# Optimization experiments

Measured on AMD Instinct MI355X. Metric: run time of the kernel, lower is better.

The kernel has to match this reference:

```python
import jax, jax.numpy as jnp
import numpy as np

BLOCK = 32          # QLinearLPBQ block_size
W_BITS = 4          # low-precision blockwise weight quantization
ACT_BITS = 16       # ActivationQDQ(bits=16)


def act_qdq(x):
    # per-tensor symmetric 16-bit fake quant-dequant (dynamic absmax scale)
    qmax = 2.0 ** (ACT_BITS - 1) - 1.0  # 32767
    scale = jnp.maximum(jnp.max(jnp.abs(x)) / qmax, 1e-12)
    return jnp.clip(jnp.round(x / scale), -qmax - 1.0, qmax) * scale


def fixed_qdq_u16(x):
    # FixedActivationQDQ: scale = 1/65536, zero_point = 0, unsigned 16-bit grid
    scale = 1.0 / 65536.0
    return jnp.clip(jnp.round(x / scale), 0.0, 65535.0) * scale


def lpbq_dequant(w):
    # blockwise (per output row, per 32-wide input block) 4-bit fake quant-dequant
    O, I = w.shape
    qmax = 2.0 ** (W_BITS - 1) - 1.0  # 7
    wb = w.reshape(O, I // BLOCK, BLOCK)
    s = jnp.maximum(jnp.max(jnp.abs(wb), axis=-1, keepdims=True) / qmax, 1e-12)
    wq = jnp.clip(jnp.round(wb / s), -qmax - 1.0, qmax) * s
    return wq.reshape(O, I)


def setup_inputs() -> dict:
    key = jax.random.key(0)
    k1, k2, k3, k4 = jax.random.split(key, 4)
    B, S, H, I = 2, 4096, 1024, 3072
    x = jax.random.normal(k1, (B, S, H), jnp.float32)
    w_gate = jax.random.normal(k2, (I, H), jnp.float32) * 0.02
    w_up = jax.random.normal(k3, (I, H), jnp.float32) * 0.02
    w_down = jax.random.normal(k4, (H, I), jnp.float32) * 0.02
    return {"x": x, "w_gate": w_gate, "w_up": w_up, "w_down": w_down}


def reference(x, w_gate, w_up, w_down):
    # x: [B, S, H]
    x = act_qdq(x)                                        # up_proj_input_qdq
    up = act_qdq(x @ lpbq_dequant(w_up).T)                # up_proj + output qdq -> [B,S,I]
    gate = act_qdq(x @ lpbq_dequant(w_gate).T)            # gate_proj + output qdq
    sig = fixed_qdq_u16(jax.nn.sigmoid(gate))             # sigmoid on fixed u16 grid
    gate = act_qdq(gate * sig)                            # SiLU (x*sigmoid) + qdq
    o = act_qdq(gate * up)                                # down_proj_input_qdq
    return o @ lpbq_dequant(w_down).T                     # [B, S, H]
```

## Files before the change

kernel.cpp:

```cpp
#include <hip/hip_runtime.h>
#include <hip/hip_bf16.h>
#include <stdint.h>


#define M_ROWS 8192
#define H_DIM 1024
#define I_DIM 3072

typedef unsigned short u16;
typedef unsigned int u32;
typedef __attribute__((ext_vector_type(8))) short bf16x8;
typedef __attribute__((ext_vector_type(4))) float f32x4;

#define WAITVM(n) asm volatile("s_waitcnt vmcnt(" #n ")" ::: "memory")
#define BAR()                                   \
  do {                                          \
    asm volatile("" ::: "memory");              \
    __builtin_amdgcn_s_barrier();               \
    asm volatile("" ::: "memory");              \
  } while (0)

__device__ __forceinline__ float bf2f(u16 v) { return __uint_as_float(((u32)v) << 16); }
__device__ __forceinline__ u16 f2bf(float f) {
  u32 u = __float_as_uint(f);
  u32 r = (u + 0x7fffu + ((u >> 16) & 1u)) >> 16;
  return (u16)r;
}
__device__ __forceinline__ float qdq16i(float x, float inv, float s) {
  float q = rintf(x * inv);
  q = fminf(fmaxf(q, -32768.f), 32767.f);
  return q * s;
}
__device__ __forceinline__ float sigq(float g) {
  float sig = __builtin_amdgcn_rcpf(1.f + __expf(-g));
  return fminf(fmaxf(rintf(sig * 65536.f), 0.f), 65535.f) * (1.f / 65536.f);
}

__device__ __forceinline__ float scale_read(const u32* __restrict__ scal, int s) {
  u32 m = 0;
#pragma unroll
  for (int j = 0; j < 16; ++j) m = max(m, scal[j * 16 + s]);
  return fmaxf(__uint_as_float(m) / 32767.f, 1e-12f);
}

__device__ __forceinline__ void load_lds16(const u16* g, u16* lds) {
  __builtin_amdgcn_global_load_lds(
      (const __attribute__((address_space(1))) u32*)g,
      (__attribute__((address_space(3))) u32*)lds, 16, 0, 0);
}

__device__ __forceinline__ void block_amax_atomic(float mx, u32* scal, int s) {
#pragma unroll
  for (int off = 32; off; off >>= 1) mx = fmaxf(mx, __shfl_xor(mx, off));
  __shared__ float red[4];
  const int lane = threadIdx.x & 63, wave = threadIdx.x >> 6;
  if (lane == 0) red[wave] = mx;
  __syncthreads();
  if (threadIdx.x == 0) {
    float m = fmaxf(fmaxf(red[0], red[1]), fmaxf(red[2], red[3]));
    atomicMax(scal + (blockIdx.x & 15) * 16 + s, __float_as_uint(m));
  }
}

__device__ __forceinline__ void block_amax4(float a, float b, float c, float d,
                                            u32* __restrict__ scal) {
#pragma unroll
  for (int off = 32; off; off >>= 1) {
    a = fmaxf(a, __shfl_xor(a, off));
    b = fmaxf(b, __shfl_xor(b, off));
    c = fmaxf(c, __shfl_xor(c, off));
    d = fmaxf(d, __shfl_xor(d, off));
  }
  __shared__ float red4[4][4];
  const int lane = threadIdx.x & 63, wave = threadIdx.x >> 6;
  if (lane == 0) {
    red4[0][wave] = a;
    red4[1][wave] = b;
    red4[2][wave] = c;
    red4[3][wave] = d;
  }
  __syncthreads();
  if (threadIdx.x == 0) {
    u32* base = scal + (blockIdx.x & 15) * 16;
#pragma unroll
    for (int s = 0; s < 4; ++s) {
      float m = fmaxf(fmaxf(red4[s][0], red4[s][1]), fmaxf(red4[s][2], red4[s][3]));
      atomicMax(base + 1 + s, __float_as_uint(m));
    }
  }
}

__global__ void __launch_bounds__(256, 2) kgemm1(const u16* __restrict__ xq,
                                                 const u16* __restrict__ wcat,
                                                 u16* __restrict__ up, u16* __restrict__ gh,
                                                 u32* __restrict__ scal) {
  __shared__ __align__(16) u16 smem[36864];
  const int tileN = blockIdx.x * 128;
  const int tileM = blockIdx.y * 128;
  const int tid = threadIdx.x;
  const int lane = tid & 63, wave = tid >> 6;
  const int wm = wave >> 1, wn = wave & 1;
  const int quad = lane >> 4, mrow = lane & 15;

  const u16* Ablk = xq + (size_t)tileM * H_DIM;
  const u16* Bublk = wcat + (size_t)tileN * H_DIM;
  const u16* Bgblk = wcat + (size_t)(I_DIM + tileN) * H_DIM;

  int goff[2], loff[2];
#pragma unroll
  for (int t = 0; t < 2; ++t) {
    const int c = tid + 256 * t;
    const int r = c >> 2, q = c & 3;
    goff[t] = r * H_DIM + ((q ^ ((r >> 1) & 3)) << 3);
    loff[t] = c << 3;
  }
  const int pc = (quad ^ ((mrow >> 1) & 3)) << 3;
  int aoff[4], boff[4];
#pragma unroll
  for (int i = 0; i < 4; ++i) {
    aoff[i] = (wm * 64 + i * 16 + mrow) * 32 + pc;
    boff[i] = (wn * 64 + i * 16 + mrow) * 32 + pc;
  }

  f32x4 accg[4][4], accu[4][4];
#pragma unroll
  for (int i = 0; i < 4; ++i)
#pragma unroll
    for (int j = 0; j < 4; ++j) {
      accg[i][j] = (f32x4){0.f, 0.f, 0.f, 0.f};
      accu[i][j] = (f32x4){0.f, 0.f, 0.f, 0.f};
    }

  auto stage = [&](int k0, int bb) {
    u16* d = smem + bb;
#pragma unroll
    for (int t = 0; t < 2; ++t) load_lds16(Ablk + k0 + goff[t], d + loff[t]);
#pragma unroll
    for (int t = 0; t < 2; ++t) load_lds16(Bublk + k0 + goff[t], d + 4096 + loff[t]);
#pragma unroll
    for (int t = 0; t < 2; ++t) load_lds16(Bgblk + k0 + goff[t], d + 8192 + loff[t]);
  };
  auto compute = [&](int bb) {
    const u16* As = smem + bb;
    const u16* Bus = As + 4096;
    const u16* Bgs = As + 8192;
    bf16x8 af[4];
#pragma unroll
    for (int i = 0; i < 4; ++i) af[i] = *(const bf16x8*)&As[aoff[i]];
#pragma unroll
    for (int j = 0; j < 4; ++j) {
      bf16x8 b = *(const bf16x8*)&Bus[boff[j]];
#pragma unroll
      for (int i = 0; i < 4; ++i)
        accu[i][j] = __builtin_amdgcn_mfma_f32_16x16x32_bf16(af[i], b, accu[i][j], 0, 0, 0);
    }
#pragma unroll
    for (int j = 0; j < 4; ++j) {
      bf16x8 b = *(const bf16x8*)&Bgs[boff[j]];
#pragma unroll
      for (int i = 0; i < 4; ++i)
        accg[i][j] = __builtin_amdgcn_mfma_f32_16x16x32_bf16(af[i], b, accg[i][j], 0, 0, 0);
    }
  };

  stage(0, 0);
  stage(32, 12288);
  stage(64, 24576);
  WAITVM(12);
  BAR();

  int bb = 0;
#pragma unroll 1
  for (int t = 0; t < 29; ++t) {
    compute(bb);
    BAR();
    stage((t + 3) * 32, bb);
    WAITVM(12);
    BAR();
    bb = (bb == 24576) ? 0 : bb + 12288;
  }
  compute(bb); BAR(); WAITVM(6); BAR(); bb = (bb == 24576) ? 0 : bb + 12288;
  compute(bb); BAR(); WAITVM(0); BAR(); bb = (bb == 24576) ? 0 : bb + 12288;
  compute(bb);

  const int rb = (lane >> 4) * 4, cb = lane & 15;
  const int erow = lane >> 2, echk = lane & 3;
  u16* gstage = smem + wave * 1152;
  u16* ustage = smem + 12288 + wave * 1152;
  const u16* grb = gstage + erow * 72;
  const u16* urb = ustage + erow * 72;
  float mxg = 0.f, mxu = 0.f, mxh = 0.f, mxo = 0.f;
#pragma unroll
  for (int i = 0; i < 4; ++i) {
    __syncthreads();
#pragma unroll
    for (int j = 0; j < 4; ++j)
#pragma unroll
      for (int r = 0; r < 4; ++r) {
        float g = accg[i][j][r];
        float u = accu[i][j][r];
        mxg = fmaxf(mxg, fabsf(g));
        mxu = fmaxf(mxu, fabsf(u));
        float ha = g * sigq(g);
        mxh = fmaxf(mxh, fabsf(ha));
        mxo = fmaxf(mxo, fabsf(ha * u));
        gstage[(rb + r) * 72 + j * 16 + cb] = f2bf(g);
        ustage[(rb + r) * 72 + j * 16 + cb] = f2bf(u);
      }
    __syncthreads();
    uint4 g0 = *(const uint4*)(grb + echk * 8);
    uint4 g1 = *(const uint4*)(grb + (echk + 4) * 8);
    uint4 u0 = *(const uint4*)(urb + echk * 8);
    uint4 u1 = *(const uint4*)(urb + (echk + 4) * 8);
    size_t grow = (size_t)(tileM + wm * 64 + i * 16 + erow) * I_DIM + (tileN + wn * 64);
    *(uint4*)(gh + grow + echk * 8) = g0;
    *(uint4*)(gh + grow + (echk + 4) * 8) = g1;
    *(uint4*)(up + grow + echk * 8) = u0;
    *(uint4*)(up + grow + (echk + 4) * 8) = u1;
  }
  block_amax4(mxu, mxg, mxh, mxo, scal);
}

__global__ void __launch_bounds__(256, 2) kgemm2(const u16* __restrict__ oq,
                                                 const u16* __restrict__ wdq,
                                                 float* __restrict__ out) {
  __shared__ __align__(16) u16 smem[32768];
  const int tileN = blockIdx.x * 128;
  const int tileM = blockIdx.y * 128;
  const int tid = threadIdx.x;
  const int lane = tid & 63, wave = tid >> 6;
  const int wm = wave >> 1, wn = wave & 1;
  const int quad = lane >> 4, mrow = lane & 15;

  const u16* Ablk = oq + (size_t)tileM * I_DIM;
  const u16* Bblk = wdq + (size_t)tileN * I_DIM;

  int goff[2], loff[2];
#pragma unroll
  for (int t = 0; t < 2; ++t) {
    const int c = tid + 256 * t;
    const int r = c >> 2, q = c & 3;
    goff[t] = r * I_DIM + ((q ^ ((r >> 1) & 3)) << 3);
    loff[t] = c << 3;
  }
  const int pc = (quad ^ ((mrow >> 1) & 3)) << 3;
  int aoff[4], boff[4];
#pragma unroll
  for (int i = 0; i < 4; ++i) {
    aoff[i] = (wm * 64 + i * 16 + mrow) * 32 + pc;
    boff[i] = (wn * 64 + i * 16 + mrow) * 32 + pc;
  }

  f32x4 acc[4][4];
#pragma unroll
  for (int i = 0; i < 4; ++i)
#pragma unroll
    for (int j = 0; j < 4; ++j) acc[i][j] = (f32x4){0.f, 0.f, 0.f, 0.f};

  auto stage = [&](int k0, int bb) {
    u16* d = smem + bb;
#pragma unroll
    for (int t = 0; t < 2; ++t) load_lds16(Ablk + k0 + goff[t], d + loff[t]);
#pragma unroll
    for (int t = 0; t < 2; ++t) load_lds16(Bblk + k0 + goff[t], d + 4096 + loff[t]);
  };
  auto compute = [&](int bb) {
    const u16* As = smem + bb;
    const u16* Bs = As + 4096;
    bf16x8 af[4];
#pragma unroll
    for (int i = 0; i < 4; ++i) af[i] = *(const bf16x8*)&As[aoff[i]];
#pragma unroll
    for (int j = 0; j < 4; ++j) {
      bf16x8 b = *(const bf16x8*)&Bs[boff[j]];
#pragma unroll
      for (int i = 0; i < 4; ++i)
        acc[i][j] = __builtin_amdgcn_mfma_f32_16x16x32_bf16(af[i], b, acc[i][j], 0, 0, 0);
    }
  };

  stage(0, 0);
  stage(32, 8192);
  stage(64, 16384);
  stage(96, 24576);
  WAITVM(12);
  BAR();

  int bb = 0;
#pragma unroll 1
  for (int t = 0; t < 92; ++t) {
    compute(bb);
    BAR();
    stage((t + 4) * 32, bb);
    WAITVM(12);
    BAR();
    bb = (bb + 8192) & 32767;
  }
  compute(bb); BAR(); WAITVM(8); BAR(); bb = (bb + 8192) & 32767;
  compute(bb); BAR(); WAITVM(4); BAR(); bb = (bb + 8192) & 32767;
  compute(bb); BAR(); WAITVM(0); BAR(); bb = (bb + 8192) & 32767;
  compute(bb);

  const int rb = (lane >> 4) * 4, cb = lane & 15;
#pragma unroll
  for (int i = 0; i < 4; ++i) {
#pragma unroll
    for (int j = 0; j < 4; ++j) {
      size_t base = (size_t)(tileM + wm * 64 + i * 16 + rb) * H_DIM +
                    (size_t)(tileN + wn * 64 + j * 16 + cb);
#pragma unroll
      for (int r = 0; r < 4; ++r) out[base + (size_t)r * H_DIM] = acc[i][j][r];
    }
  }
}

__global__ void __launch_bounds__(256) kprep(const float* __restrict__ x,
                                             const float* __restrict__ wu,
                                             const float* __restrict__ wg,
                                             const float* __restrict__ wdn,
                                             u16* __restrict__ wcat, u16* __restrict__ wdq,
                                             u32* __restrict__ scal) {
  if (blockIdx.x < 1024) {
    const float4* x4 = (const float4*)x;
    const int n4 = (M_ROWS * H_DIM) / 4;
    float mx = 0.f;
    for (int i = blockIdx.x * 256 + threadIdx.x; i < n4; i += 1024 * 256) {
      float4 v = x4[i];
      mx = fmaxf(fmaxf(fabsf(v.x), fabsf(v.y)), fmaxf(fmaxf(fabsf(v.z), fabsf(v.w)), mx));
    }
    block_amax_atomic(mx, scal, 0);
    return;
  }
  const int gid = (blockIdx.x - 1024) * 256 + threadIdx.x;
  const int unit = gid >> 3, l8 = gid & 7;
  const float* src;
  u16* dst;
  int u;
  if (unit < 98304)       { src = wu;  dst = wcat;            u = unit; }
  else if (unit < 196608) { src = wg;  dst = wcat + 3145728;  u = unit - 98304; }
  else                    { src = wdn; dst = wdq;             u = unit - 196608; }
  const size_t off = (size_t)u * 32 + (size_t)l8 * 4;
  float4 v = *(const float4*)(src + off);
  float m = fmaxf(fmaxf(fabsf(v.x), fabsf(v.y)), fmaxf(fabsf(v.z), fabsf(v.w)));
  m = fmaxf(m, __shfl_xor(m, 1));
  m = fmaxf(m, __shfl_xor(m, 2));
  m = fmaxf(m, __shfl_xor(m, 4));
  const float s = fmaxf(m / 7.0f, 1e-12f);
  const float inv = 1.0f / s;
  float vv[4] = {v.x, v.y, v.z, v.w};
  u16 o[4];
#pragma unroll
  for (int e = 0; e < 4; ++e) {
    float q = rintf(vv[e] * inv);
    q = fminf(fmaxf(q, -8.f), 7.f);
    o[e] = f2bf(q * s);
  }
  *(ushort4*)(dst + off) = make_ushort4(o[0], o[1], o[2], o[3]);
}

__global__ void __launch_bounds__(256) kqdqx(const float4* __restrict__ x,
                                             ushort4* __restrict__ xq,
                                             const u32* __restrict__ scal) {
  const float s = scale_read(scal, 0);
  const float inv = 1.0f / s;
  const int i = blockIdx.x * 256 + threadIdx.x;
  float4 v = x[i];
  ushort4 o;
  o.x = f2bf(qdq16i(v.x, inv, s));
  o.y = f2bf(qdq16i(v.y, inv, s));
  o.z = f2bf(qdq16i(v.z, inv, s));
  o.w = f2bf(qdq16i(v.w, inv, s));
  xq[i] = o;
}

#define GH4 ((M_ROWS * I_DIM) / 8)
#define EW_BLOCKS 2048

__global__ void __launch_bounds__(256) kmulo(uint4* __restrict__ gh, const uint4* __restrict__ up,
                                             u32* __restrict__ scal) {
  const float sg = scale_read(scal, 2), ig = 1.0f / sg;
  const float sh = scale_read(scal, 3), ih = 1.0f / sh;
  const float su = scale_read(scal, 1), iu = 1.0f / su;
  const float so = scale_read(scal, 4), io = 1.0f / so;
  for (int i = blockIdx.x * 256 + threadIdx.x; i < GH4; i += EW_BLOCKS * 256) {
    union { uint4 v; u16 us[8]; } a, b;
    a.v = gh[i];
    b.v = up[i];
#pragma unroll
    for (int e = 0; e < 8; ++e) {
      float g = qdq16i(bf2f(a.us[e]), ig, sg);
      float h = g * sigq(g);
      float o = qdq16i(h, ih, sh) * qdq16i(bf2f(b.us[e]), iu, su);
      a.us[e] = f2bf(qdq16i(o, io, so));
    }
    gh[i] = a.v;
  }
}

extern "C" void kernel_launch(void* const* d_in, const int* in_sizes, int n_in,
                              void* d_out, int out_size, void* d_ws, size_t ws_size,
                              hipStream_t stream) {
  (void)in_sizes; (void)n_in; (void)out_size; (void)ws_size;
  const float* x   = (const float*)d_in[0];
  const float* wg  = (const float*)d_in[1];
  const float* wu  = (const float*)d_in[2];
  const float* wdn = (const float*)d_in[3];
  float* out = (float*)d_out;
  char* ws = (char*)d_ws;

  u32* scal = (u32*)ws;
  u16* xq   = (u16*)(ws + 1024);
  u16* wcat = xq + (size_t)M_ROWS * H_DIM;
  u16* wdq  = wcat + (size_t)2 * I_DIM * H_DIM;
  u16* up   = wdq + (size_t)H_DIM * I_DIM;
  u16* gh   = up + (size_t)M_ROWS * I_DIM;

  hipMemsetAsync(scal, 0, 1024, stream);
  kprep<<<1024 + 9216, 256, 0, stream>>>(x, wu, wg, wdn, wcat, wdq, scal);
  kqdqx<<<(M_ROWS * H_DIM) / 4 / 256, 256, 0, stream>>>((const float4*)x, (ushort4*)xq, scal);
  kgemm1<<<dim3(24, 64), 256, 0, stream>>>(xq, wcat, up, gh, scal);
  kmulo<<<EW_BLOCKS, 256, 0, stream>>>((uint4*)gh, (const uint4*)up, scal);
  kgemm2<<<dim3(8, 64), 256, 0, stream>>>(gh, wdq, out);
}
```

Measured before the change: 323.1 us.

## Interleave up/gate weights and use 256x256 tiles with 8 waves in gemm1

The up and gate weight rows are interleaved in 16-row groups, so gemm1 runs as a single 256x256-tile GEMM over the combined 6144-wide output using 512 threads. This doubles A-tile reuse and halves the number of blocks. The intermediate is stored as one interleaved buffer, and the elementwise kernel and gemm2's A loads are remapped to read the interleaved layout in place. The larger LDS footprint and the 128 accumulator floats per thread may lower occupancy or cause register spills.

```diff
diff --git a/kernel.cpp b/kernel.cpp
--- a/kernel.cpp
+++ b/kernel.cpp
@@ -62,8 +62,8 @@
   }
 }
 
-__device__ __forceinline__ void block_amax4(float a, float b, float c, float d,
-                                            u32* __restrict__ scal) {
+__device__ __forceinline__ void block_amax4_8w(float a, float b, float c, float d,
+                                               u32* __restrict__ scal) {
 #pragma unroll
   for (int off = 32; off; off >>= 1) {
     a = fmaxf(a, __shfl_xor(a, off));
@@ -71,7 +71,7 @@
     c = fmaxf(c, __shfl_xor(c, off));
     d = fmaxf(d, __shfl_xor(d, off));
   }
-  __shared__ float red4[4][4];
+  __shared__ float red4[4][8];
   const int lane = threadIdx.x & 63, wave = threadIdx.x >> 6;
   if (lane == 0) {
     red4[0][wave] = a;
@@ -84,89 +84,76 @@
     u32* base = scal + (blockIdx.x & 15) * 16;
 #pragma unroll
     for (int s = 0; s < 4; ++s) {
-      float m = fmaxf(fmaxf(red4[s][0], red4[s][1]), fmaxf(red4[s][2], red4[s][3]));
+      float m = 0.f;
+#pragma unroll
+      for (int w = 0; w < 8; ++w) m = fmaxf(m, red4[s][w]);
       atomicMax(base + 1 + s, __float_as_uint(m));
     }
   }
 }
 
-__global__ void __launch_bounds__(256, 2) kgemm1(const u16* __restrict__ xq,
+__global__ void __launch_bounds__(512, 2) kgemm1(const u16* __restrict__ xq,
                                                  const u16* __restrict__ wcat,
-                                                 u16* __restrict__ up, u16* __restrict__ gh,
+                                                 u16* __restrict__ gu,
                                                  u32* __restrict__ scal) {
-  __shared__ __align__(16) u16 smem[36864];
-  const int tileN = blockIdx.x * 128;
-  const int tileM = blockIdx.y * 128;
+  __shared__ __align__(16) u16 smem[49152];
+  const int tileN = blockIdx.x * 256;
+  const int tileM = blockIdx.y * 256;
   const int tid = threadIdx.x;
   const int lane = tid & 63, wave = tid >> 6;
-  const int wm = wave >> 1, wn = wave & 1;
+  const int wm = wave >> 2, wn = wave & 3;
   const int quad = lane >> 4, mrow = lane & 15;
 
   const u16* Ablk = xq + (size_t)tileM * H_DIM;
-  const u16* Bublk = wcat + (size_t)tileN * H_DIM;
-  const u16* Bgblk = wcat + (size_t)(I_DIM + tileN) * H_DIM;
+  const u16* Bblk = wcat + (size_t)tileN * H_DIM;
 
   int goff[2], loff[2];
 #pragma unroll
   for (int t = 0; t < 2; ++t) {
-    const int c = tid + 256 * t;
+    const int c = tid + 512 * t;
     const int r = c >> 2, q = c & 3;
     goff[t] = r * H_DIM + ((q ^ ((r >> 1) & 3)) << 3);
     loff[t] = c << 3;
   }
   const int pc = (quad ^ ((mrow >> 1) & 3)) << 3;
-  int aoff[4], boff[4];
-#pragma unroll
-  for (int i = 0; i < 4; ++i) {
-    aoff[i] = (wm * 64 + i * 16 + mrow) * 32 + pc;
-    boff[i] = (wn * 64 + i * 16 + mrow) * 32 + pc;
-  }
-
-  f32x4 accg[4][4], accu[4][4];
-#pragma unroll
-  for (int i = 0; i < 4; ++i)
-#pragma unroll
-    for (int j = 0; j < 4; ++j) {
-      accg[i][j] = (f32x4){0.f, 0.f, 0.f, 0.f};
-      accu[i][j] = (f32x4){0.f, 0.f, 0.f, 0.f};
-    }
+  int arow[8], brow[4];
+#pragma unroll
+  for (int i = 0; i < 8; ++i) arow[i] = (wm * 128 + i * 16 + mrow) * 32 + pc;
+#pragma unroll
+  for (int j = 0; j < 4; ++j) brow[j] = (wn * 64 + j * 16 + mrow) * 32 + pc;
+
+  f32x4 acc[8][4];
+#pragma unroll
+  for (int i = 0; i < 8; ++i)
+#pragma unroll
+    for (int j = 0; j < 4; ++j) acc[i][j] = (f32x4){0.f, 0.f, 0.f, 0.f};
 
   auto stage = [&](int k0, int bb) {
     u16* d = smem + bb;
 #pragma unroll
     for (int t = 0; t < 2; ++t) load_lds16(Ablk + k0 + goff[t], d + loff[t]);
 #pragma unroll
-    for (int t = 0; t < 2; ++t) load_lds16(Bublk + k0 + goff[t], d + 4096 + loff[t]);
-#pragma unroll
-    for (int t = 0; t < 2; ++t) load_lds16(Bgblk + k0 + goff[t], d + 8192 + loff[t]);
+    for (int t = 0; t < 2; ++t) load_lds16(Bblk + k0 + goff[t], d + 8192 + loff[t]);
   };
   auto compute = [&](int bb) {
     const u16* As = smem + bb;
-    const u16* Bus = As + 4096;
-    const u16* Bgs = As + 8192;
-    bf16x8 af[4];
-#pragma unroll
-    for (int i = 0; i < 4; ++i) af[i] = *(const bf16x8*)&As[aoff[i]];
+    const u16* Bs = As + 8192;
+    bf16x8 af[8];
+#pragma unroll
+    for (int i = 0; i < 8; ++i) af[i] = *(const bf16x8*)&As[arow[i]];
 #pragma unroll
     for (int j = 0; j < 4; ++j) {
-      bf16x8 b = *(const bf16x8*)&Bus[boff[j]];
-#pragma unroll
-      for (int i = 0; i < 4; ++i)
-        accu[i][j] = __builtin_amdgcn_mfma_f32_16x16x32_bf16(af[i], b, accu[i][j], 0, 0, 0);
-    }
-#pragma unroll
-    for (int j = 0; j < 4; ++j) {
-      bf16x8 b = *(const bf16x8*)&Bgs[boff[j]];
-#pragma unroll
-      for (int i = 0; i < 4; ++i)
-        accg[i][j] = __builtin_amdgcn_mfma_f32_16x16x32_bf16(af[i], b, accg[i][j], 0, 0, 0);
+      bf16x8 b = *(const bf16x8*)&Bs[brow[j]];
+#pragma unroll
+      for (int i = 0; i < 8; ++i)
+        acc[i][j] = __builtin_amdgcn_mfma_f32_16x16x32_bf16(af[i], b, acc[i][j], 0, 0, 0);
     }
   };
 
   stage(0, 0);
-  stage(32, 12288);
-  stage(64, 24576);
-  WAITVM(12);
+  stage(32, 16384);
+  stage(64, 32768);
+  WAITVM(8);
   BAR();
 
   int bb = 0;
@@ -175,53 +162,48 @@
     compute(bb);
     BAR();
     stage((t + 3) * 32, bb);
-    WAITVM(12);
+    WAITVM(8);
     BAR();
-    bb = (bb == 24576) ? 0 : bb + 12288;
-  }
-  compute(bb); BAR(); WAITVM(6); BAR(); bb = (bb == 24576) ? 0 : bb + 12288;
-  compute(bb); BAR(); WAITVM(0); BAR(); bb = (bb == 24576) ? 0 : bb + 12288;
+    bb = (bb == 32768) ? 0 : bb + 16384;
+  }
+  compute(bb); BAR(); WAITVM(4); BAR(); bb = (bb == 32768) ? 0 : bb + 16384;
+  compute(bb); BAR(); WAITVM(0); BAR(); bb = (bb == 32768) ? 0 : bb + 16384;
   compute(bb);
 
   const int rb = (lane >> 4) * 4, cb = lane & 15;
   const int erow = lane >> 2, echk = lane & 3;
-  u16* gstage = smem + wave * 1152;
-  u16* ustage = smem + 12288 + wave * 1152;
-  const u16* grb = gstage + erow * 72;
-  const u16* urb = ustage + erow * 72;
+  u16* wstage = smem + wave * 1152;
+  const u16* wrb = wstage + erow * 72;
   float mxg = 0.f, mxu = 0.f, mxh = 0.f, mxo = 0.f;
 #pragma unroll
-  for (int i = 0; i < 4; ++i) {
+  for (int i = 0; i < 8; ++i) {
     __syncthreads();
 #pragma unroll
-    for (int j = 0; j < 4; ++j)
+    for (int jp = 0; jp < 4; jp += 2)
 #pragma unroll
       for (int r = 0; r < 4; ++r) {
-        float g = accg[i][j][r];
-        float u = accu[i][j][r];
+        float u = acc[i][jp][r];
+        float g = acc[i][jp + 1][r];
+        mxu = fmaxf(mxu, fabsf(u));
         mxg = fmaxf(mxg, fabsf(g));
-        mxu = fmaxf(mxu, fabsf(u));
         float ha = g * sigq(g);
         mxh = fmaxf(mxh, fabsf(ha));
         mxo = fmaxf(mxo, fabsf(ha * u));
-        gstage[(rb + r) * 72 + j * 16 + cb] = f2bf(g);
-        ustage[(rb + r) * 72 + j * 16 + cb] = f2bf(u);
+        wstage[(rb + r) * 72 + jp * 16 + cb] = f2bf(u);
+        wstage[(rb + r) * 72 + (jp + 1) * 16 + cb] = f2bf(g);
       }
     __syncthreads();
-    uint4 g0 = *(const uint4*)(grb + echk * 8);
-    uint4 g1 = *(const uint4*)(grb + (echk + 4) * 8);
-    uint4 u0 = *(const uint4*)(urb + echk * 8);
-    uint4 u1 = *(const uint4*)(urb + (echk + 4) * 8);
-    size_t grow = (size_t)(tileM + wm * 64 + i * 16 + erow) * I_DIM + (tileN + wn * 64);
-    *(uint4*)(gh + grow + echk * 8) = g0;
-    *(uint4*)(gh + grow + (echk + 4) * 8) = g1;
-    *(uint4*)(up + grow + echk * 8) = u0;
-    *(uint4*)(up + grow + (echk + 4) * 8) = u1;
-  }
-  block_amax4(mxu, mxg, mxh, mxo, scal);
-}
-
-__global__ void __launch_bounds__(256, 2) kgemm2(const u16* __restrict__ oq,
+    uint4 v0 = *(const uint4*)(wrb + echk * 8);
+    uint4 v1 = *(const uint4*)(wrb + (echk + 4) * 8);
+    size_t grow = (size_t)(tileM + wm * 128 + i * 16 + erow) * (2 * I_DIM) +
+                  (tileN + wn * 64);
+    *(uint4*)(gu + grow + echk * 8) = v0;
+    *(uint4*)(gu + grow + (echk + 4) * 8) = v1;
+  }
+  block_amax4_8w(mxu, mxg, mxh, mxo, scal);
+}
+
+__global__ void __launch_bounds__(256, 2) kgemm2(const u16* __restrict__ gu,
                                                  const u16* __restrict__ wdq,
                                                  float* __restrict__ out) {
   __shared__ __align__(16) u16 smem[32768];
@@ -232,15 +214,17 @@
   const int wm = wave >> 1, wn = wave & 1;
   const int quad = lane >> 4, mrow = lane & 15;
 
-  const u16* Ablk = oq + (size_t)tileM * I_DIM;
+  const u16* Ablk = gu + (size_t)tileM * (2 * I_DIM);
   const u16* Bblk = wdq + (size_t)tileN * I_DIM;
 
-  int goff[2], loff[2];
+  int goffA[2], goffB[2], loff[2];
 #pragma unroll
   for (int t = 0; t < 2; ++t) {
     const int c = tid + 256 * t;
     const int r = c >> 2, q = c & 3;
-    goff[t] = r * I_DIM + ((q ^ ((r >> 1) & 3)) << 3);
+    const int l = q ^ ((r >> 1) & 3);
+    goffA[t] = r * (2 * I_DIM) + ((l >> 1) << 5) + ((l & 1) << 3);
+    goffB[t] = r * I_DIM + (l << 3);
     loff[t] = c << 3;
   }
   const int pc = (quad ^ ((mrow >> 1) & 3)) << 3;
@@ -260,9 +244,9 @@
   auto stage = [&](int k0, int bb) {
     u16* d = smem + bb;
 #pragma unroll
-    for (int t = 0; t < 2; ++t) load_lds16(Ablk + k0 + goff[t], d + loff[t]);
-#pragma unroll
-    for (int t = 0; t < 2; ++t) load_lds16(Bblk + k0 + goff[t], d + 4096 + loff[t]);
+    for (int t = 0; t < 2; ++t) load_lds16(Ablk + 2 * k0 + goffA[t], d + loff[t]);
+#pragma unroll
+    for (int t = 0; t < 2; ++t) load_lds16(Bblk + k0 + goffB[t], d + 4096 + loff[t]);
   };
   auto compute = [&](int bb) {
     const u16* As = smem + bb;
@@ -335,12 +319,23 @@
   const int unit = gid >> 3, l8 = gid & 7;
   const float* src;
   u16* dst;
-  int u;
-  if (unit < 98304)       { src = wu;  dst = wcat;            u = unit; }
-  else if (unit < 196608) { src = wg;  dst = wcat + 3145728;  u = unit - 98304; }
-  else                    { src = wdn; dst = wdq;             u = unit - 196608; }
-  const size_t off = (size_t)u * 32 + (size_t)l8 * 4;
-  float4 v = *(const float4*)(src + off);
+  size_t soff, doff;
+  if (unit < 196608) {
+    const int head = unit < 98304 ? 0 : 1;
+    const int u = head ? unit - 98304 : unit;
+    src = head ? wg : wu;
+    dst = wcat;
+    const int c = u >> 5, blk = u & 31;
+    const int n = ((c >> 4) << 5) + (head << 4) + (c & 15);
+    soff = (size_t)u * 32 + l8 * 4;
+    doff = (size_t)n * 1024 + blk * 32 + l8 * 4;
+  } else {
+    const int u = unit - 196608;
+    src = wdn;
+    dst = wdq;
+    soff = doff = (size_t)u * 32 + l8 * 4;
+  }
+  float4 v = *(const float4*)(src + soff);
   float m = fmaxf(fmaxf(fabsf(v.x), fabsf(v.y)), fmaxf(fabsf(v.z), fabsf(v.w)));
   m = fmaxf(m, __shfl_xor(m, 1));
   m = fmaxf(m, __shfl_xor(m, 2));
@@ -355,7 +350,7 @@
     q = fminf(fmaxf(q, -8.f), 7.f);
     o[e] = f2bf(q * s);
   }
-  *(ushort4*)(dst + off) = make_ushort4(o[0], o[1], o[2], o[3]);
+  *(ushort4*)(dst + doff) = make_ushort4(o[0], o[1], o[2], o[3]);
 }
 
 __global__ void __launch_bounds__(256) kqdqx(const float4* __restrict__ x,
@@ -373,27 +368,36 @@
   xq[i] = o;
 }
 
-#define GH4 ((M_ROWS * I_DIM) / 8)
 #define EW_BLOCKS 2048
 
-__global__ void __launch_bounds__(256) kmulo(uint4* __restrict__ gh, const uint4* __restrict__ up,
+__global__ void __launch_bounds__(256) kmulo(uint4* __restrict__ gu4,
                                              u32* __restrict__ scal) {
   const float sg = scale_read(scal, 2), ig = 1.0f / sg;
   const float sh = scale_read(scal, 3), ih = 1.0f / sh;
   const float su = scale_read(scal, 1), iu = 1.0f / su;
   const float so = scale_read(scal, 4), io = 1.0f / so;
-  for (int i = blockIdx.x * 256 + threadIdx.x; i < GH4; i += EW_BLOCKS * 256) {
-    union { uint4 v; u16 us[8]; } a, b;
-    a.v = gh[i];
-    b.v = up[i];
+  const int NG = M_ROWS * 192;
+  for (int idx = blockIdx.x * 256 + threadIdx.x; idx < NG; idx += EW_BLOCKS * 256) {
+    const int m = idx / 192, b = idx - m * 192;
+    const int i0 = m * 768 + b * 4;
+    union { uint4 v; u16 us[8]; } u0, u1, g0, g1;
+    u0.v = gu4[i0];
+    u1.v = gu4[i0 + 1];
+    g0.v = gu4[i0 + 2];
+    g1.v = gu4[i0 + 3];
 #pragma unroll
     for (int e = 0; e < 8; ++e) {
-      float g = qdq16i(bf2f(a.us[e]), ig, sg);
+      float g = qdq16i(bf2f(g0.us[e]), ig, sg);
       float h = g * sigq(g);
-      float o = qdq16i(h, ih, sh) * qdq16i(bf2f(b.us[e]), iu, su);
-      a.us[e] = f2bf(qdq16i(o, io, so));
-    }
-    gh[i] = a.v;
+      float o = qdq16i(h, ih, sh) * qdq16i(bf2f(u0.us[e]), iu, su);
+      u0.us[e] = f2bf(qdq16i(o, io, so));
+      float g2 = qdq16i(bf2f(g1.us[e]), ig, sg);
+      float h2 = g2 * sigq(g2);
+      float o2 = qdq16i(h2, ih, sh) * qdq16i(bf2f(u1.us[e]), iu, su);
+      u1.us[e] = f2bf(qdq16i(o2, io, so));
+    }
+    gu4[i0] = u0.v;
+    gu4[i0 + 1] = u1.v;
   }
 }
 
@@ -412,13 +416,12 @@
   u16* xq   = (u16*)(ws + 1024);
   u16* wcat = xq + (size_t)M_ROWS * H_DIM;
   u16* wdq  = wcat + (size_t)2 * I_DIM * H_DIM;
-  u16* up   = wdq + (size_t)H_DIM * I_DIM;
-  u16* gh   = up + (size_t)M_ROWS * I_DIM;
+  u16* gu   = wdq + (size_t)H_DIM * I_DIM;
 
   hipMemsetAsync(scal, 0, 1024, stream);
   kprep<<<1024 + 9216, 256, 0, stream>>>(x, wu, wg, wdn, wcat, wdq, scal);
   kqdqx<<<(M_ROWS * H_DIM) / 4 / 256, 256, 0, stream>>>((const float4*)x, (ushort4*)xq, scal);
-  kgemm1<<<dim3(24, 64), 256, 0, stream>>>(xq, wcat, up, gh, scal);
-  kmulo<<<EW_BLOCKS, 256, 0, stream>>>((uint4*)gh, (const uint4*)up, scal);
-  kgemm2<<<dim3(8, 64), 256, 0, stream>>>(gh, wdq, out);
-}
+  kgemm1<<<dim3(24, 32), 512, 0, stream>>>(xq, wcat, gu, scal);
+  kmulo<<<EW_BLOCKS, 256, 0, stream>>>((uint4*)gu, scal);
+  kgemm2<<<dim3(8, 64), 256, 0, stream>>>(gu, wdq, out);
+}
```

After: 385.7 us. +19.4%, slower.

## Enlarge down-proj GEMM tile to 256x128 with three-stage LDS pipeline

Applied to the files above, without the earlier changes.

The down-projection GEMM now computes a 256x128 output tile per block instead of 128x128, so each wave accumulates an 8x4 grid of MFMA tiles and each loaded B fragment is reused across twice as many A rows. To fit in shared memory, the LDS ring drops from four stages to three, with 24 KB per stage. The grid is halved to 256 blocks. The accumulators double to 128 floats per thread, which raises register pressure against the 2-blocks-per-SM launch bound, and the shallower prefetch may expose more memory latency. With only 256 blocks, the work may also spread unevenly across the CUs.

```diff
diff --git a/kernel.cpp b/kernel.cpp
--- a/kernel.cpp
+++ b/kernel.cpp
@@ -224,9 +224,9 @@
 __global__ void __launch_bounds__(256, 2) kgemm2(const u16* __restrict__ oq,
                                                  const u16* __restrict__ wdq,
                                                  float* __restrict__ out) {
-  __shared__ __align__(16) u16 smem[32768];
+  __shared__ __align__(16) u16 smem[36864];
   const int tileN = blockIdx.x * 128;
-  const int tileM = blockIdx.y * 128;
+  const int tileM = blockIdx.y * 256;
   const int tid = threadIdx.x;
   const int lane = tid & 63, wave = tid >> 6;
   const int wm = wave >> 1, wn = wave & 1;
@@ -235,78 +235,82 @@
   const u16* Ablk = oq + (size_t)tileM * I_DIM;
   const u16* Bblk = wdq + (size_t)tileN * I_DIM;
 
-  int goff[2], loff[2];
+  int goffA[4], loffA[4], goffB[2], loffB[2];
+#pragma unroll
+  for (int t = 0; t < 4; ++t) {
+    const int c = tid + 256 * t;
+    const int r = c >> 2, q = c & 3;
+    goffA[t] = r * I_DIM + ((q ^ ((r >> 1) & 3)) << 3);
+    loffA[t] = c << 3;
+  }
 #pragma unroll
   for (int t = 0; t < 2; ++t) {
     const int c = tid + 256 * t;
     const int r = c >> 2, q = c & 3;
-    goff[t] = r * I_DIM + ((q ^ ((r >> 1) & 3)) << 3);
-    loff[t] = c << 3;
+    goffB[t] = r * I_DIM + ((q ^ ((r >> 1) & 3)) << 3);
+    loffB[t] = c << 3;
   }
   const int pc = (quad ^ ((mrow >> 1) & 3)) << 3;
-  int aoff[4], boff[4];
-#pragma unroll
-  for (int i = 0; i < 4; ++i) {
-    aoff[i] = (wm * 64 + i * 16 + mrow) * 32 + pc;
-    boff[i] = (wn * 64 + i * 16 + mrow) * 32 + pc;
-  }
-
-  f32x4 acc[4][4];
-#pragma unroll
-  for (int i = 0; i < 4; ++i)
+  int aoff[8], boff[4];
+#pragma unroll
+  for (int i = 0; i < 8; ++i) aoff[i] = (wm * 128 + i * 16 + mrow) * 32 + pc;
+#pragma unroll
+  for (int j = 0; j < 4; ++j) boff[j] = (wn * 64 + j * 16 + mrow) * 32 + pc;
+
+  f32x4 acc[8][4];
+#pragma unroll
+  for (int i = 0; i < 8; ++i)
 #pragma unroll
     for (int j = 0; j < 4; ++j) acc[i][j] = (f32x4){0.f, 0.f, 0.f, 0.f};
 
   auto stage = [&](int k0, int bb) {
     u16* d = smem + bb;
 #pragma unroll
-    for (int t = 0; t < 2; ++t) load_lds16(Ablk + k0 + goff[t], d + loff[t]);
-#pragma unroll
-    for (int t = 0; t < 2; ++t) load_lds16(Bblk + k0 + goff[t], d + 4096 + loff[t]);
+    for (int t = 0; t < 4; ++t) load_lds16(Ablk + k0 + goffA[t], d + loffA[t]);
+#pragma unroll
+    for (int t = 0; t < 2; ++t) load_lds16(Bblk + k0 + goffB[t], d + 8192 + loffB[t]);
   };
   auto compute = [&](int bb) {
     const u16* As = smem + bb;
-    const u16* Bs = As + 4096;
-    bf16x8 af[4];
-#pragma unroll
-    for (int i = 0; i < 4; ++i) af[i] = *(const bf16x8*)&As[aoff[i]];
+    const u16* Bs = As + 8192;
+    bf16x8 af[8];
+#pragma unroll
+    for (int i = 0; i < 8; ++i) af[i] = *(const bf16x8*)&As[aoff[i]];
 #pragma unroll
     for (int j = 0; j < 4; ++j) {
       bf16x8 b = *(const bf16x8*)&Bs[boff[j]];
 #pragma unroll
-      for (int i = 0; i < 4; ++i)
+      for (int i = 0; i < 8; ++i)
         acc[i][j] = __builtin_amdgcn_mfma_f32_16x16x32_bf16(af[i], b, acc[i][j], 0, 0, 0);
     }
   };
 
   stage(0, 0);
-  stage(32, 8192);
-  stage(64, 16384);
-  stage(96, 24576);
+  stage(32, 12288);
+  stage(64, 24576);
   WAITVM(12);
   BAR();
 
   int bb = 0;
 #pragma unroll 1
-  for (int t = 0; t < 92; ++t) {
+  for (int t = 0; t < 93; ++t) {
     compute(bb);
     BAR();
-    stage((t + 4) * 32, bb);
+    stage((t + 3) * 32, bb);
     WAITVM(12);
     BAR();
-    bb = (bb + 8192) & 32767;
-  }
-  compute(bb); BAR(); WAITVM(8); BAR(); bb = (bb + 8192) & 32767;
-  compute(bb); BAR(); WAITVM(4); BAR(); bb = (bb + 8192) & 32767;
-  compute(bb); BAR(); WAITVM(0); BAR(); bb = (bb + 8192) & 32767;
+    bb = (bb == 24576) ? 0 : bb + 12288;
+  }
+  compute(bb); BAR(); WAITVM(6); BAR(); bb = (bb == 24576) ? 0 : bb + 12288;
+  compute(bb); BAR(); WAITVM(0); BAR(); bb = (bb == 24576) ? 0 : bb + 12288;
   compute(bb);
 
   const int rb = (lane >> 4) * 4, cb = lane & 15;
 #pragma unroll
-  for (int i = 0; i < 4; ++i) {
+  for (int i = 0; i < 8; ++i) {
 #pragma unroll
     for (int j = 0; j < 4; ++j) {
-      size_t base = (size_t)(tileM + wm * 64 + i * 16 + rb) * H_DIM +
+      size_t base = (size_t)(tileM + wm * 128 + i * 16 + rb) * H_DIM +
                     (size_t)(tileN + wn * 64 + j * 16 + cb);
 #pragma unroll
       for (int r = 0; r < 4; ++r) out[base + (size_t)r * H_DIM] = acc[i][j][r];
@@ -420,5 +424,5 @@
   kqdqx<<<(M_ROWS * H_DIM) / 4 / 256, 256, 0, stream>>>((const float4*)x, (ushort4*)xq, scal);
   kgemm1<<<dim3(24, 64), 256, 0, stream>>>(xq, wcat, up, gh, scal);
   kmulo<<<EW_BLOCKS, 256, 0, stream>>>((uint4*)gh, (const uint4*)up, scal);
-  kgemm2<<<dim3(8, 64), 256, 0, stream>>>(gh, wdq, out);
-}
+  kgemm2<<<dim3(8, 32), 256, 0, stream>>>(gh, wdq, out);
+}
```

New measurement: 322.9 us. Within noise of the previous version (-0.1%).

## Enlarge down-proj GEMM tile to 256x128 with 8 waves and K=64 double buffering

Applied to the files above, without the earlier changes.

Reworks kgemm2 to use 512-thread blocks computing 256x128 output tiles, which halves the grid in M and increases reuse of the B tile. The K-step grows from 32 to 64 with an 8-chunk XOR swizzle, and the 4-stage async pipeline with explicit vmcnt waits becomes a 2-stage double buffer using __syncthreads. This cuts barrier count per FLOP and global traffic for weights. In exchange it may lose latency hiding, since only one stage is in flight. LDS use rises to 96KB, which may limit occupancy to one block per CU despite the launch bound.

```diff
diff --git a/kernel.cpp b/kernel.cpp
--- a/kernel.cpp
+++ b/kernel.cpp
@@ -221,12 +221,12 @@
   block_amax4(mxu, mxg, mxh, mxo, scal);
 }
 
-__global__ void __launch_bounds__(256, 2) kgemm2(const u16* __restrict__ oq,
+__global__ void __launch_bounds__(512, 2) kgemm2(const u16* __restrict__ oq,
                                                  const u16* __restrict__ wdq,
                                                  float* __restrict__ out) {
-  __shared__ __align__(16) u16 smem[32768];
+  __shared__ __align__(16) u16 smem[49152];
   const int tileN = blockIdx.x * 128;
-  const int tileM = blockIdx.y * 128;
+  const int tileM = blockIdx.y * 256;
   const int tid = threadIdx.x;
   const int lane = tid & 63, wave = tid >> 6;
   const int wm = wave >> 1, wn = wave & 1;
@@ -235,20 +235,28 @@
   const u16* Ablk = oq + (size_t)tileM * I_DIM;
   const u16* Bblk = wdq + (size_t)tileN * I_DIM;
 
-  int goff[2], loff[2];
+  int goffA[4], loffA[4], goffB[2], loffB[2];
+#pragma unroll
+  for (int t = 0; t < 4; ++t) {
+    const int c = tid + 512 * t;
+    const int r = c >> 3, q = c & 7;
+    goffA[t] = r * I_DIM + ((q ^ (r & 7)) << 3);
+    loffA[t] = c << 3;
+  }
 #pragma unroll
   for (int t = 0; t < 2; ++t) {
-    const int c = tid + 256 * t;
-    const int r = c >> 2, q = c & 3;
-    goff[t] = r * I_DIM + ((q ^ ((r >> 1) & 3)) << 3);
-    loff[t] = c << 3;
-  }
-  const int pc = (quad ^ ((mrow >> 1) & 3)) << 3;
-  int aoff[4], boff[4];
+    const int c = tid + 512 * t;
+    const int r = c >> 3, q = c & 7;
+    goffB[t] = r * I_DIM + ((q ^ (r & 7)) << 3);
+    loffB[t] = c << 3;
+  }
+  const int pc0 = (quad ^ (mrow & 7)) << 3;
+  const int pc1 = ((quad + 4) ^ (mrow & 7)) << 3;
+  int arow[4], brow[4];
 #pragma unroll
   for (int i = 0; i < 4; ++i) {
-    aoff[i] = (wm * 64 + i * 16 + mrow) * 32 + pc;
-    boff[i] = (wn * 64 + i * 16 + mrow) * 32 + pc;
+    arow[i] = (wm * 64 + i * 16 + mrow) << 6;
+    brow[i] = (wn * 64 + i * 16 + mrow) << 6;
   }
 
   f32x4 acc[4][4];
@@ -257,49 +265,44 @@
 #pragma unroll
     for (int j = 0; j < 4; ++j) acc[i][j] = (f32x4){0.f, 0.f, 0.f, 0.f};
 
-  auto stage = [&](int k0, int bb) {
-    u16* d = smem + bb;
-#pragma unroll
-    for (int t = 0; t < 2; ++t) load_lds16(Ablk + k0 + goff[t], d + loff[t]);
-#pragma unroll
-    for (int t = 0; t < 2; ++t) load_lds16(Bblk + k0 + goff[t], d + 4096 + loff[t]);
-  };
-  auto compute = [&](int bb) {
-    const u16* As = smem + bb;
-    const u16* Bs = As + 4096;
-    bf16x8 af[4];
-#pragma unroll
-    for (int i = 0; i < 4; ++i) af[i] = *(const bf16x8*)&As[aoff[i]];
-#pragma unroll
-    for (int j = 0; j < 4; ++j) {
-      bf16x8 b = *(const bf16x8*)&Bs[boff[j]];
-#pragma unroll
-      for (int i = 0; i < 4; ++i)
-        acc[i][j] = __builtin_amdgcn_mfma_f32_16x16x32_bf16(af[i], b, acc[i][j], 0, 0, 0);
-    }
-  };
-
-  stage(0, 0);
-  stage(32, 8192);
-  stage(64, 16384);
-  stage(96, 24576);
-  WAITVM(12);
-  BAR();
-
-  int bb = 0;
-#pragma unroll 1
-  for (int t = 0; t < 92; ++t) {
-    compute(bb);
-    BAR();
-    stage((t + 4) * 32, bb);
-    WAITVM(12);
-    BAR();
-    bb = (bb + 8192) & 32767;
-  }
-  compute(bb); BAR(); WAITVM(8); BAR(); bb = (bb + 8192) & 32767;
-  compute(bb); BAR(); WAITVM(4); BAR(); bb = (bb + 8192) & 32767;
-  compute(bb); BAR(); WAITVM(0); BAR(); bb = (bb + 8192) & 32767;
-  compute(bb);
+  {
+    u16* d = smem;
+#pragma unroll
+    for (int t = 0; t < 4; ++t) load_lds16(Ablk + goffA[t], d + loffA[t]);
+#pragma unroll
+    for (int t = 0; t < 2; ++t) load_lds16(Bblk + goffB[t], d + 16384 + loffB[t]);
+  }
+  __syncthreads();
+
+  int cur = 0;
+  for (int k0 = 0; k0 < I_DIM; k0 += 64) {
+    if (k0 + 64 < I_DIM) {
+      u16* d = smem + (cur ^ 1) * 24576;
+      const int kn = k0 + 64;
+#pragma unroll
+      for (int t = 0; t < 4; ++t) load_lds16(Ablk + kn + goffA[t], d + loffA[t]);
+#pragma unroll
+      for (int t = 0; t < 2; ++t) load_lds16(Bblk + kn + goffB[t], d + 16384 + loffB[t]);
+    }
+    const u16* As = smem + cur * 24576;
+    const u16* Bs = As + 16384;
+#pragma unroll
+    for (int kk = 0; kk < 2; ++kk) {
+      const int pc = kk ? pc1 : pc0;
+      bf16x8 af[4];
+#pragma unroll
+      for (int t = 0; t < 4; ++t) af[t] = *(const bf16x8*)&As[arow[t] + pc];
+#pragma unroll
+      for (int j = 0; j < 4; ++j) {
+        bf16x8 b = *(const bf16x8*)&Bs[brow[j] + pc];
+#pragma unroll
+        for (int i = 0; i < 4; ++i)
+          acc[i][j] = __builtin_amdgcn_mfma_f32_16x16x32_bf16(af[i], b, acc[i][j], 0, 0, 0);
+      }
+    }
+    __syncthreads();
+    cur ^= 1;
+  }
 
   const int rb = (lane >> 4) * 4, cb = lane & 15;
 #pragma unroll
@@ -420,5 +423,5 @@
   kqdqx<<<(M_ROWS * H_DIM) / 4 / 256, 256, 0, stream>>>((const float4*)x, (ushort4*)xq, scal);
   kgemm1<<<dim3(24, 64), 256, 0, stream>>>(xq, wcat, up, gh, scal);
   kmulo<<<EW_BLOCKS, 256, 0, stream>>>((uint4*)gh, (const uint4*)up, scal);
-  kgemm2<<<dim3(8, 64), 256, 0, stream>>>(gh, wdq, out);
-}
+  kgemm2<<<dim3(8, 32), 512, 0, stream>>>(gh, wdq, out);
+}
```

After: 321.2 us. No clear change (-0.6%).
